# Kernel tuning notes

Hardware: AMD Instinct MI355X
Metric: run time of the kernel (lower is better)

Reference implementation:

```python
import jax, jax.numpy as jnp
import numpy as np

TAIL_BOUND = 3.0
MIN_BIN_WIDTH = 1e-3
MIN_BIN_HEIGHT = 1e-3
SEARCH_EPS = 1e-6


def setup_inputs() -> dict:
    key = jax.random.key(0)
    k1, k2, k3, k4, k5 = jax.random.split(key, 5)
    B, D, K = 8192, 256, 8
    return {
        "x": jax.random.normal(k1, (B, D), dtype=jnp.float32),
        "w_": jax.random.normal(k2, (B, D, K), dtype=jnp.float32),
        "h_": jax.random.normal(k3, (B, D, K), dtype=jnp.float32),
        "dl_": jax.random.normal(k4, (B, D, 1), dtype=jnp.float32),
        "dr_": jax.random.normal(k5, (B, D, 1), dtype=jnp.float32),
    }


def _cumknots(unnorm, min_bin):
    # softmax -> min-width floor -> cumsum with exact 0/1 endpoints
    num_bins = unnorm.shape[-1]
    w = jax.nn.softmax(unnorm, axis=-1)
    w = min_bin + (1.0 - min_bin * num_bins) * w
    cum = jnp.cumsum(w, axis=-1)
    cum = cum.at[..., -1].set(1.0)
    pad = [(0, 0)] * (cum.ndim - 1) + [(1, 0)]
    cum = jnp.pad(cum, pad)
    return w, cum


def reference(x, w_, h_, dl_, dr_):
    num_bins = w_.shape[-1]
    left = bottom = -TAIL_BOUND
    right = top = TAIL_BOUND

    inside = (x >= left) & (x <= right)

    # map to unit interval; clamp keeps masked-out lanes numerically safe
    t = jnp.clip((x - left) / (right - left), 0.0, 1.0)

    widths, cumwidths = _cumknots(w_, MIN_BIN_WIDTH)       # [B,D,K], [B,D,K+1]
    heights, cumheights = _cumknots(h_, MIN_BIN_HEIGHT)

    slopes = heights / widths                              # [B,D,K]
    min1 = jnp.minimum(jnp.abs(slopes[..., :-1]), jnp.abs(slopes[..., 1:]))
    min2 = 0.5 * (widths[..., 1:] * slopes[..., :-1] + widths[..., :-1] * slopes[..., 1:]) \
           / (widths[..., :-1] + widths[..., 1:])
    mins = jnp.minimum(min1, min2)                         # [B,D,K-1]

    d_left = jax.nn.sigmoid(dl_) * 3.0 * slopes[..., :1]
    d_right = jax.nn.sigmoid(dr_) * 3.0 * slopes[..., -1:]
    d_mid = mins * (jnp.sign(slopes[..., :-1]) + jnp.sign(slopes[..., 1:]))
    derivs = jnp.concatenate([d_left, d_mid, d_right], axis=-1)  # [B,D,K+1]

    a = (derivs[..., :-1] + derivs[..., 1:] - 2.0 * slopes) / widths ** 2
    b = (3.0 * slopes - 2.0 * derivs[..., :-1] - derivs[..., 1:]) / widths
    c = derivs[..., :-1]
    d = cumheights[..., :-1]

    # searchsorted: sum(t >= knots) - 1, with eps bump on the last knot
    knots = cumwidths.at[..., -1].add(SEARCH_EPS)
    bin_idx = jnp.sum((t[..., None] >= knots).astype(jnp.int32), axis=-1) - 1
    bin_idx = jnp.clip(bin_idx, 0, num_bins - 1)[..., None]  # [B,D,1]

    take = lambda arr: jnp.take_along_axis(arr, bin_idx, axis=-1)[..., 0]
    ia, ib, ic, id_ = take(a), take(b), take(c), take(d)
    lw = take(cumwidths)

    sx = t - lw
    out_s = ia * sx ** 3 + ib * sx ** 2 + ic * sx + id_
    lad_s = jnp.log(jnp.abs(3.0 * ia * sx ** 2 + 2.0 * ib * sx + ic))

    out_s = jnp.clip(out_s, 0.0, 1.0) * (top - bottom) + bottom
    lad_s = lad_s + jnp.log(top - bottom) - jnp.log(right - left)

    outputs = jnp.where(inside, out_s, x)          # identity tails
    logabsdet = jnp.where(inside, lad_s, 0.0)
    return outputs, logabsdet
```

## Files before the change

kernel.cpp:

```cpp
#include <hip/hip_runtime.h>
#include <math.h>


constexpr int K = 8;
constexpr float TAIL = 3.0f;
constexpr float MIN_BIN = 0.001f;
constexpr float SEARCH_EPS = 1e-6f;

__device__ __forceinline__ float rcpf(float v) {
    return __builtin_amdgcn_rcpf(v);
}

__global__ __launch_bounds__(256) void cbs_kernel(
    const float* __restrict__ x_,
    const float* __restrict__ w_,
    const float* __restrict__ h_,
    const float* __restrict__ dl_,
    const float* __restrict__ dr_,
    float* __restrict__ out,
    float* __restrict__ lad,
    int n)
{
    const int tid    = blockIdx.x * blockDim.x + threadIdx.x;
    const int stride = gridDim.x * blockDim.x;

    float4 nwa, nwb, nha, nhb;
    float  nx, ndl, ndr;

    int j = tid;
    if (j < n) {
        const float4* w4 = (const float4*)w_ + 2 * (size_t)j;
        const float4* h4 = (const float4*)h_ + 2 * (size_t)j;
        nwa = w4[0]; nwb = w4[1];
        nha = h4[0]; nhb = h4[1];
        nx  = x_[j]; ndl = dl_[j]; ndr = dr_[j];
    }

    while (j < n) {
        const float4 wa = nwa, wb = nwb, ha = nha, hb = nhb;
        const float  xv = nx, dlv = ndl, drv = ndr;
        const int cur = j;
        j += stride;

        if (j < n) {
            const float4* w4 = (const float4*)w_ + 2 * (size_t)j;
            const float4* h4 = (const float4*)h_ + 2 * (size_t)j;
            nwa = w4[0]; nwb = w4[1];
            nha = h4[0]; nhb = h4[1];
            nx  = x_[j]; ndl = dl_[j]; ndr = dr_[j];
        }

        float wr[K] = {wa.x, wa.y, wa.z, wa.w, wb.x, wb.y, wb.z, wb.w};
        float hr[K] = {ha.x, ha.y, ha.z, ha.w, hb.x, hb.y, hb.z, hb.w};

        float sw = 0.0f;
        #pragma unroll
        for (int k = 0; k < K; k++) { wr[k] = __expf(wr[k]); sw += wr[k]; }
        float cs = (1.0f - MIN_BIN * K) * rcpf(sw);
        #pragma unroll
        for (int k = 0; k < K; k++) wr[k] = MIN_BIN + cs * wr[k];

        float sh = 0.0f;
        #pragma unroll
        for (int k = 0; k < K; k++) { hr[k] = __expf(hr[k]); sh += hr[k]; }
        float csh = (1.0f - MIN_BIN * K) * rcpf(sh);
        #pragma unroll
        for (int k = 0; k < K; k++) hr[k] = MIN_BIN + csh * hr[k];

        float cw[K + 1]; cw[0] = 0.0f;
        #pragma unroll
        for (int k = 0; k < K; k++) cw[k + 1] = cw[k] + wr[k];
        float ch[K + 1]; ch[0] = 0.0f;
        #pragma unroll
        for (int k = 0; k < K; k++) ch[k + 1] = ch[k] + hr[k];

        float s[K];
        #pragma unroll
        for (int k = 0; k < K; k++) s[k] = hr[k] * rcpf(wr[k]);

        float dv[K + 1];
        dv[0] = rcpf(1.0f + __expf(-dlv)) * 3.0f * s[0];
        dv[K] = rcpf(1.0f + __expf(-drv)) * 3.0f * s[K - 1];
        #pragma unroll
        for (int k = 0; k < K - 1; k++) {
            float two_m1 = 2.0f * fminf(s[k], s[k + 1]);
            float m2x = (wr[k + 1] * s[k] + wr[k] * s[k + 1])
                        * rcpf(wr[k] + wr[k + 1]);
            dv[k + 1] = fminf(two_m1, m2x);
        }

        float t = (xv + TAIL) * (1.0f / (2.0f * TAIL));
        t = fminf(fmaxf(t, 0.0f), 1.0f);

        int bin = 0;
        #pragma unroll
        for (int jj = 1; jj < K; jj++) bin += (t >= cw[jj]) ? 1 : 0;
        bin += (t >= 1.0f + SEARCH_EPS) ? 1 : 0;
        if (bin > K - 1) bin = K - 1;

        float wk = wr[0], sk = s[0], d0 = dv[0], d1 = dv[1], lw = cw[0], dd = ch[0];
        #pragma unroll
        for (int k = 1; k < K; k++) {
            bool sel = (bin == k);
            wk = sel ? wr[k]     : wk;
            sk = sel ? s[k]      : sk;
            d0 = sel ? dv[k]     : d0;
            d1 = sel ? dv[k + 1] : d1;
            lw = sel ? cw[k]     : lw;
            dd = sel ? ch[k]     : dd;
        }

        float inv_wk = rcpf(wk);
        float ia = (d0 + d1 - 2.0f * sk) * inv_wk * inv_wk;
        float ib = (3.0f * sk - 2.0f * d0 - d1) * inv_wk;
        float ic = d0;

        float sx = t - lw;
        float out_s = ((ia * sx + ib) * sx + ic) * sx + dd;
        float der   = (3.0f * ia * sx + 2.0f * ib) * sx + ic;
        float lad_s = __logf(fabsf(der));

        out_s = fminf(fmaxf(out_s, 0.0f), 1.0f) * (2.0f * TAIL) - TAIL;

        bool inside = (xv >= -TAIL) && (xv <= TAIL);
        __builtin_nontemporal_store(inside ? out_s : xv,   out + cur);
        __builtin_nontemporal_store(inside ? lad_s : 0.0f, lad + cur);
    }
}

extern "C" void kernel_launch(void* const* d_in, const int* in_sizes, int n_in,
                              void* d_out, int out_size, void* d_ws, size_t ws_size,
                              hipStream_t stream) {
    const float* x  = (const float*)d_in[0];
    const float* w  = (const float*)d_in[1];
    const float* h  = (const float*)d_in[2];
    const float* dl = (const float*)d_in[3];
    const float* dr = (const float*)d_in[4];
    int n = in_sizes[0];
    float* out = (float*)d_out;
    float* lad = out + n;

    const int threads = 256;
    const int blocks  = 2048;
    cbs_kernel<<<blocks, threads, 0, stream>>>(x, w, h, dl, dr, out, lad, n);
}
```

Measured before the change: 180.3 us.

## Process four elements per thread with vectorized loads and stores, no grid-stride loop

Replaces the grid-stride loop with software prefetch by a one-shot kernel in which each thread handles four contiguous elements. It loads 16 float4 vectors of w/h up front, reads x/dl/dr as float4, and writes outputs as float4 nontemporal stores. The grid is sized to cover n exactly. This puts more loads in flight per thread and widens the x/dl/dr/out accesses, at the cost of higher register pressure. It assumes n is a multiple of 4 and has no tail handling.

Measured after the change: 187.7 us. 4.1% more time.

```diff
diff --git a/kernel.cpp b/kernel.cpp
--- a/kernel.cpp
+++ b/kernel.cpp
@@ -3,9 +3,12 @@
 
 
 constexpr int K = 8;
+constexpr int E = 4;
 constexpr float TAIL = 3.0f;
 constexpr float MIN_BIN = 0.001f;
 constexpr float SEARCH_EPS = 1e-6f;
+
+typedef float vfloat4 __attribute__((ext_vector_type(4)));
 
 __device__ __forceinline__ float rcpf(float v) {
     return __builtin_amdgcn_rcpf(v);
@@ -21,37 +24,30 @@
     float* __restrict__ lad,
     int n)
 {
-    const int tid    = blockIdx.x * blockDim.x + threadIdx.x;
-    const int stride = gridDim.x * blockDim.x;
+    const int t  = blockIdx.x * blockDim.x + threadIdx.x;
+    const int e0 = t * E;
+    if (e0 >= n) return;
 
-    float4 nwa, nwb, nha, nhb;
-    float  nx, ndl, ndr;
+    const vfloat4* w4 = (const vfloat4*)w_ + 2 * (size_t)e0;
+    const vfloat4* h4 = (const vfloat4*)h_ + 2 * (size_t)e0;
+    vfloat4 wv[2 * E], hv[2 * E];
+    #pragma unroll
+    for (int q = 0; q < 2 * E; q++) wv[q] = w4[q];
+    #pragma unroll
+    for (int q = 0; q < 2 * E; q++) hv[q] = h4[q];
+    vfloat4 xv4  = ((const vfloat4*)x_)[t];
+    vfloat4 dl4  = ((const vfloat4*)dl_)[t];
+    vfloat4 dr4  = ((const vfloat4*)dr_)[t];
 
-    int j = tid;
-    if (j < n) {
-        const float4* w4 = (const float4*)w_ + 2 * (size_t)j;
-        const float4* h4 = (const float4*)h_ + 2 * (size_t)j;
-        nwa = w4[0]; nwb = w4[1];
-        nha = h4[0]; nhb = h4[1];
-        nx  = x_[j]; ndl = dl_[j]; ndr = dr_[j];
-    }
+    float outs[E], lads[E];
 
-    while (j < n) {
-        const float4 wa = nwa, wb = nwb, ha = nha, hb = nhb;
-        const float  xv = nx, dlv = ndl, drv = ndr;
-        const int cur = j;
-        j += stride;
-
-        if (j < n) {
-            const float4* w4 = (const float4*)w_ + 2 * (size_t)j;
-            const float4* h4 = (const float4*)h_ + 2 * (size_t)j;
-            nwa = w4[0]; nwb = w4[1];
-            nha = h4[0]; nhb = h4[1];
-            nx  = x_[j]; ndl = dl_[j]; ndr = dr_[j];
-        }
-
-        float wr[K] = {wa.x, wa.y, wa.z, wa.w, wb.x, wb.y, wb.z, wb.w};
-        float hr[K] = {ha.x, ha.y, ha.z, ha.w, hb.x, hb.y, hb.z, hb.w};
+    #pragma unroll
+    for (int e = 0; e < E; e++) {
+        float wr[K] = {wv[2*e].x, wv[2*e].y, wv[2*e].z, wv[2*e].w,
+                       wv[2*e+1].x, wv[2*e+1].y, wv[2*e+1].z, wv[2*e+1].w};
+        float hr[K] = {hv[2*e].x, hv[2*e].y, hv[2*e].z, hv[2*e].w,
+                       hv[2*e+1].x, hv[2*e+1].y, hv[2*e+1].z, hv[2*e+1].w};
+        const float xv = xv4[e], dlv = dl4[e], drv = dr4[e];
 
         float sw = 0.0f;
         #pragma unroll
@@ -89,13 +85,13 @@
             dv[k + 1] = fminf(two_m1, m2x);
         }
 
-        float t = (xv + TAIL) * (1.0f / (2.0f * TAIL));
-        t = fminf(fmaxf(t, 0.0f), 1.0f);
+        float tt = (xv + TAIL) * (1.0f / (2.0f * TAIL));
+        tt = fminf(fmaxf(tt, 0.0f), 1.0f);
 
         int bin = 0;
         #pragma unroll
-        for (int jj = 1; jj < K; jj++) bin += (t >= cw[jj]) ? 1 : 0;
-        bin += (t >= 1.0f + SEARCH_EPS) ? 1 : 0;
+        for (int jj = 1; jj < K; jj++) bin += (tt >= cw[jj]) ? 1 : 0;
+        bin += (tt >= 1.0f + SEARCH_EPS) ? 1 : 0;
         if (bin > K - 1) bin = K - 1;
 
         float wk = wr[0], sk = s[0], d0 = dv[0], d1 = dv[1], lw = cw[0], dd = ch[0];
@@ -115,7 +111,7 @@
         float ib = (3.0f * sk - 2.0f * d0 - d1) * inv_wk;
         float ic = d0;
 
-        float sx = t - lw;
+        float sx = tt - lw;
         float out_s = ((ia * sx + ib) * sx + ic) * sx + dd;
         float der   = (3.0f * ia * sx + 2.0f * ib) * sx + ic;
         float lad_s = __logf(fabsf(der));
@@ -123,9 +119,14 @@
         out_s = fminf(fmaxf(out_s, 0.0f), 1.0f) * (2.0f * TAIL) - TAIL;
 
         bool inside = (xv >= -TAIL) && (xv <= TAIL);
-        __builtin_nontemporal_store(inside ? out_s : xv,   out + cur);
-        __builtin_nontemporal_store(inside ? lad_s : 0.0f, lad + cur);
+        outs[e] = inside ? out_s : xv;
+        lads[e] = inside ? lad_s : 0.0f;
     }
+
+    vfloat4 o4 = {outs[0], outs[1], outs[2], outs[3]};
+    vfloat4 l4 = {lads[0], lads[1], lads[2], lads[3]};
+    __builtin_nontemporal_store(o4, (vfloat4*)out + t);
+    __builtin_nontemporal_store(l4, (vfloat4*)lad + t);
 }
 
 extern "C" void kernel_launch(void* const* d_in, const int* in_sizes, int n_in,
@@ -141,6 +142,7 @@
     float* lad = out + n;
 
     const int threads = 256;
-    const int blocks  = 2048;
+    const int per_block = threads * E;
+    const int blocks = (n + per_block - 1) / per_block;
     cbs_kernel<<<blocks, threads, 0, stream>>>(x, w, h, dl, dr, out, lad, n);
 }
```
